# Optimization experiments

Hardware: AMD Instinct MI355X
Metric: run time of the kernel (lower is better)

The kernel has to match this reference:

```python
import jax, jax.numpy as jnp
import numpy as np

N_NODES = 50000
N_EDGES = 800000
N_FEAT = 100
HIDDEN = 100
N_CLASSES = 2
N_GRAPHS = 256


def setup_inputs() -> dict:
    key = jax.random.key(0)
    ks = jax.random.split(key, 16)
    x = jax.random.normal(ks[0], (N_NODES, N_FEAT), dtype=jnp.float32)
    edge_index = jax.random.randint(ks[1], (2, N_EDGES), 0, N_NODES, dtype=jnp.int64)
    batch = jnp.sort(jax.random.randint(ks[2], (N_NODES,), 0, N_GRAPHS, dtype=jnp.int64))
    def lin(k, fan_in, fan_out):
        s = 1.0 / np.sqrt(fan_in)
        return jax.random.uniform(k, (fan_in, fan_out), jnp.float32, -s, s)
    return {
        "x": x, "edge_index": edge_index, "batch": batch,
        # SAGEConv1: lin_l (neighbor aggr, with bias), lin_r (root, no bias)
        "W1l": lin(ks[3], N_FEAT, HIDDEN), "b1": jnp.zeros((HIDDEN,), jnp.float32), "W1r": lin(ks[4], N_FEAT, HIDDEN),
        "W2l": lin(ks[5], HIDDEN, HIDDEN), "b2": jnp.zeros((HIDDEN,), jnp.float32), "W2r": lin(ks[6], HIDDEN, HIDDEN),
        "W3l": lin(ks[7], HIDDEN, HIDDEN), "b3": jnp.zeros((HIDDEN,), jnp.float32), "W3r": lin(ks[8], HIDDEN, HIDDEN),
        "Wlin": lin(ks[9], HIDDEN, N_CLASSES), "blin": jnp.zeros((N_CLASSES,), jnp.float32),
    }


def _sage_conv(x, src, dst, Wl, b, Wr):
    # PyG SAGEConv with mean aggregation: out = lin_l(mean_{j in N(i)} x_j) + lin_r(x_i)
    msg = x[src]  # [E, d] gather
    s = jax.ops.segment_sum(msg, dst, num_segments=x.shape[0])  # [N, d]
    cnt = jax.ops.segment_sum(jnp.ones_like(dst, dtype=x.dtype), dst, num_segments=x.shape[0])
    aggr = s / jnp.maximum(cnt, 1.0)[:, None]
    return aggr @ Wl + b + x @ Wr


def reference(x, edge_index, batch, W1l, b1, W1r, W2l, b2, W2r, W3l, b3, W3r, Wlin, blin):
    src, dst = edge_index[0], edge_index[1]
    h = jax.nn.relu(_sage_conv(x, src, dst, W1l, b1, W1r))
    h = jax.nn.relu(_sage_conv(h, src, dst, W2l, b2, W2r))
    h = _sage_conv(h, src, dst, W3l, b3, W3r)
    # global_mean_pool over batch ids
    gs = jax.ops.segment_sum(h, batch, num_segments=N_GRAPHS)
    gc = jax.ops.segment_sum(jnp.ones_like(batch, dtype=h.dtype), batch, num_segments=N_GRAPHS)
    g = gs / jnp.maximum(gc, 1.0)[:, None]
    # dropout(p=0.5) is identity in eval mode
    return g @ Wlin + blin
```

## Files before the change

kernel.cpp:

```cpp
#include <hip/hip_runtime.h>
#include <hip/hip_bf16.h>

typedef __attribute__((ext_vector_type(8))) short short8v;
typedef __attribute__((ext_vector_type(4))) float f32x4;

#define PST 128
#define PSTL 136
#define MAXBUCK 1024

static __device__ inline unsigned short f2bf(float x) {
    union { float f; unsigned int u; } c; c.f = x;
    unsigned int r = (c.u + 0x7FFFu + ((c.u >> 16) & 1u)) >> 16;
    return (unsigned short)r;
}
static __device__ inline float bf2f(unsigned short h) {
    union { float f; unsigned int u; } c; c.u = ((unsigned int)h) << 16;
    return c.f;
}
static __device__ inline f32x4 MF(short8v a, short8v b, f32x4 c) {
    return __builtin_amdgcn_mfma_f32_16x16x32_bf16(a, b, c, 0, 0, 0);
}


__global__ __launch_bounds__(256) void k_bincount(const int* __restrict__ dst,
                                                  int* __restrict__ bcnt,
                                                  int n, int nbuck, int chunk) {
    __shared__ int lcnt[MAXBUCK];
    int t = threadIdx.x;
    for (int b = t; b < nbuck; b += 256) lcnt[b] = 0;
    __syncthreads();
    int e0 = blockIdx.x * chunk;
    int e1 = e0 + chunk; if (e1 > n) e1 = n;
    for (int e = e0 + t; e < e1; e += 256) atomicAdd(&lcnt[dst[e] >> 8], 1);
    __syncthreads();
    for (int b = t; b < nbuck; b += 256)
        if (lcnt[b]) atomicAdd(&bcnt[b], lcnt[b]);
}

__global__ __launch_bounds__(1024) void k_binscan(const int* __restrict__ bcnt,
                                                  int* __restrict__ bbase,
                                                  int* __restrict__ bcur,
                                                  int* __restrict__ rowp,
                                                  int nbuck, int n_nodes, int n_edges) {
    __shared__ int tmp[1024];
    int t = threadIdx.x;
    int v = (t < nbuck) ? bcnt[t] : 0;
    tmp[t] = v;
    __syncthreads();
    for (int off = 1; off < 1024; off <<= 1) {
        int u = 0;
        if (t >= off) u = tmp[t - off];
        __syncthreads();
        if (t >= off) tmp[t] += u;
        __syncthreads();
    }
    if (t < nbuck) { int b = tmp[t] - v; bbase[t] = b; bcur[t] = b; }
    if (t == 0) rowp[n_nodes] = n_edges;
}

__global__ __launch_bounds__(256) void k_binscatter(const int* __restrict__ src,
                                                    const int* __restrict__ dst,
                                                    int* __restrict__ bcur,
                                                    int* __restrict__ tmpv,
                                                    int n, int nbuck, int chunk) {
    __shared__ int lcnt[MAXBUCK];
    __shared__ int lbase[MAXBUCK];
    int t = threadIdx.x;
    for (int b = t; b < nbuck; b += 256) lcnt[b] = 0;
    __syncthreads();
    int e0 = blockIdx.x * chunk;
    int e1 = e0 + chunk; if (e1 > n) e1 = n;
    for (int e = e0 + t; e < e1; e += 256) atomicAdd(&lcnt[dst[e] >> 8], 1);
    __syncthreads();
    for (int b = t; b < nbuck; b += 256) {
        int c = lcnt[b];
        lbase[b] = c ? atomicAdd(&bcur[b], c) : 0;
        lcnt[b] = 0;
    }
    __syncthreads();
    for (int e = e0 + t; e < e1; e += 256) {
        int d = dst[e];
        int b = d >> 8;
        int r = atomicAdd(&lcnt[b], 1);
        tmpv[lbase[b] + r] = (src[e] << 8) | (d & 255);
    }
}

__global__ __launch_bounds__(256) void k_build(const int* __restrict__ tmpv,
                                               const int* __restrict__ bbase,
                                               int* __restrict__ rowp,
                                               float* __restrict__ inv,
                                               int* __restrict__ ssrc,
                                               int n_nodes, int n_edges, int nbuck) {
    __shared__ int hist[256];
    __shared__ int scan[256];
    __shared__ int curs[256];
    int b = blockIdx.x;
    int t = threadIdx.x;
    int s = bbase[b];
    int e = (b + 1 < nbuck) ? bbase[b + 1] : n_edges;
    hist[t] = 0;
    __syncthreads();
    for (int i = s + t; i < e; i += 256) atomicAdd(&hist[tmpv[i] & 255], 1);
    __syncthreads();
    int v = hist[t];
    scan[t] = v;
    __syncthreads();
    for (int off = 1; off < 256; off <<= 1) {
        int u = 0;
        if (t >= off) u = scan[t - off];
        __syncthreads();
        if (t >= off) scan[t] += u;
        __syncthreads();
    }
    int excl = scan[t] - v;
    curs[t] = excl;
    int node = (b << 8) + t;
    if (node < n_nodes) {
        rowp[node] = s + excl;
        inv[node] = 1.0f / (float)(v > 1 ? v : 1);
    }
    __syncthreads();
    for (int i = s + t; i < e; i += 256) {
        int p = tmpv[i];
        int r = atomicAdd(&curs[p & 255], 1);
        ssrc[s + r] = p >> 8;
    }
}

__global__ __launch_bounds__(256) void k_cvt(const float* __restrict__ X,
                                             unsigned short* __restrict__ Xhi,
                                             unsigned short* __restrict__ Xlo,
                                             int n) {
    int grp = threadIdx.x >> 4, l = threadIdx.x & 15;
    int i = blockIdx.x * 16 + grp;
    if (i >= n) return;
    unsigned short* ph = Xhi + (size_t)i * PST + l * 8;
    unsigned short* pl = Xlo + (size_t)i * PST + l * 8;
    if (l < 13) {
        float4 v0 = *(const float4*)(X + (size_t)i * 100 + l * 8);
        float4 v1 = (l < 12) ? *(const float4*)(X + (size_t)i * 100 + l * 8 + 4)
                             : make_float4(0.f, 0.f, 0.f, 0.f);
        float f[8] = {v0.x, v0.y, v0.z, v0.w, v1.x, v1.y, v1.z, v1.w};
        short8v hv, lv;
#pragma unroll
        for (int m = 0; m < 8; ++m) {
            unsigned short h = f2bf(f[m]);
            hv[m] = (short)h;
            lv[m] = (short)f2bf(f[m] - bf2f(h));
        }
        *(short8v*)ph = hv;
        *(short8v*)pl = lv;
    } else {
        short8v z = (short8v){0,0,0,0,0,0,0,0};
        *(short8v*)ph = z;
        *(short8v*)pl = z;
    }
}

#define PACKN (2 * 4 * 7 * 64)
__global__ __launch_bounds__(256) void k_pack3(const float* __restrict__ W1l, const float* __restrict__ W1r,
                                               const float* __restrict__ W2l, const float* __restrict__ W2r,
                                               const float* __restrict__ W3l, const float* __restrict__ W3r,
                                               unsigned short* __restrict__ B1h, unsigned short* __restrict__ B1l,
                                               unsigned short* __restrict__ B2h, unsigned short* __restrict__ B2l,
                                               unsigned short* __restrict__ B3h, unsigned short* __restrict__ B3l) {
    int gid = blockIdx.x * 256 + threadIdx.x;
    if (gid >= 3 * PACKN) return;
    int layer = gid / PACKN;
    int idx = gid - layer * PACKN;
    const float* Wl = layer == 0 ? W1l : (layer == 1 ? W2l : W3l);
    const float* Wr = layer == 0 ? W1r : (layer == 1 ? W2r : W3r);
    unsigned short* Bh = layer == 0 ? B1h : (layer == 1 ? B2h : B3h);
    unsigned short* Bl = layer == 0 ? B1l : (layer == 1 ? B2l : B3l);
    int lane = idx & 63;
    int t = idx >> 6;
    int nt = t % 7;
    int pc = t / 7;
    int part = pc >> 2, c = pc & 3;
    int col = nt * 16 + (lane & 15);
    int fbase = c * 32 + (lane >> 4) * 8;
    const float* W = part ? Wr : Wl;
    for (int jj = 0; jj < 8; ++jj) {
        int k = fbase + jj;
        float w = (k < 100 && col < 100) ? W[k * 100 + col] : 0.f;
        unsigned short h = f2bf(w);
        Bh[(size_t)idx * 8 + jj] = h;
        Bl[(size_t)idx * 8 + jj] = f2bf(w - bf2f(h));
    }
}

__global__ __launch_bounds__(128) void k_layer(const unsigned short* __restrict__ Xhi,
                                               const unsigned short* __restrict__ Xlo,
                                               const int* __restrict__ ssrc,
                                               const int* __restrict__ rowp,
                                               const float* __restrict__ inv,
                                               const unsigned short* __restrict__ Bh,
                                               const unsigned short* __restrict__ Bl,
                                               const float* __restrict__ bias,
                                               unsigned short* __restrict__ Ohi,
                                               unsigned short* __restrict__ Olo,
                                               int relu, int n) {
    __shared__ unsigned short lds_h[32][PSTL];
    __shared__ unsigned short lds_l[32][PSTL];
    const int t = threadIdx.x;
    const int wv = t >> 6;
    const int lane = t & 63;
    const int base = blockIdx.x * 32;

    {
        const int grp = lane >> 4, l = lane & 15;
        const bool act = l < 13;
        const size_t loff = (size_t)l * 8;
        const short8v z = (short8v){0,0,0,0,0,0,0,0};
#pragma unroll
        for (int it = 0; it < 4; ++it) {
            const int lr = wv * 16 + it * 4 + grp;
            const int node = base + lr;
            if (node < n) {
                int s = rowp[node];
                int e = rowp[node + 1];
                float a[8];
#pragma unroll
                for (int m = 0; m < 8; ++m) a[m] = 0.f;
                int i = s;
                for (; i + 4 <= e; i += 4) {
                    int s0 = ssrc[i], s1 = ssrc[i + 1], s2 = ssrc[i + 2], s3 = ssrc[i + 3];
                    if (act) {
                        short8v v0 = *(const short8v*)(Xhi + (size_t)s0 * PST + loff);
                        short8v v1 = *(const short8v*)(Xhi + (size_t)s1 * PST + loff);
                        short8v v2 = *(const short8v*)(Xhi + (size_t)s2 * PST + loff);
                        short8v v3 = *(const short8v*)(Xhi + (size_t)s3 * PST + loff);
#pragma unroll
                        for (int m = 0; m < 8; ++m)
                            a[m] += bf2f((unsigned short)v0[m]) + bf2f((unsigned short)v1[m])
                                  + bf2f((unsigned short)v2[m]) + bf2f((unsigned short)v3[m]);
                    }
                }
                for (; i < e; ++i) {
                    int s0 = ssrc[i];
                    if (act) {
                        short8v v0 = *(const short8v*)(Xhi + (size_t)s0 * PST + loff);
#pragma unroll
                        for (int m = 0; m < 8; ++m) a[m] += bf2f((unsigned short)v0[m]);
                    }
                }
                if (act) {
                    const float f = inv[node];
                    short8v hv, lv;
#pragma unroll
                    for (int m = 0; m < 8; ++m) {
                        float v = a[m] * f;
                        unsigned short h = f2bf(v);
                        hv[m] = (short)h;
                        lv[m] = (short)f2bf(v - bf2f(h));
                    }
                    *(short8v*)&lds_h[lr][l * 8] = hv;
                    *(short8v*)&lds_l[lr][l * 8] = lv;
                } else {
                    *(short8v*)&lds_h[lr][l * 8] = z;
                    *(short8v*)&lds_l[lr][l * 8] = z;
                }
            } else {
                *(short8v*)&lds_h[lr][l * 8] = z;
                *(short8v*)&lds_l[lr][l * 8] = z;
            }
        }
    }
    __builtin_amdgcn_wave_barrier();

    const int m0 = base + wv * 16;
    const int lrow = lane & 15;
    const int lg = lane >> 4;
    const int ldr = wv * 16 + lrow;

    f32x4 acc[7];
#pragma unroll
    for (int nt = 0; nt < 7; ++nt) acc[nt] = (f32x4){0.f, 0.f, 0.f, 0.f};

    int r0 = m0 + lrow; if (r0 >= n) r0 = n - 1;
    const size_t b0 = (size_t)r0 * PST + lg * 8;

#pragma unroll
    for (int c = 0; c < 4; ++c) {
        short8v ah0 = *(const short8v*)&lds_h[ldr][c * 32 + lg * 8];
        short8v al0 = *(const short8v*)&lds_l[ldr][c * 32 + lg * 8];
        const unsigned short* bph = Bh + ((size_t)(c * 7) * 64 + lane) * 8;
        const unsigned short* bpl = Bl + ((size_t)(c * 7) * 64 + lane) * 8;
#pragma unroll
        for (int nt = 0; nt < 7; ++nt) {
            short8v bh = *(const short8v*)(bph + nt * 512);
            short8v bl = *(const short8v*)(bpl + nt * 512);
            acc[nt] = MF(ah0, bh, acc[nt]);
            acc[nt] = MF(ah0, bl, acc[nt]);
            acc[nt] = MF(al0, bh, acc[nt]);
        }
    }
#pragma unroll
    for (int c = 0; c < 4; ++c) {
        short8v ah0 = *(const short8v*)(Xhi + b0 + c * 32);
        short8v al0 = *(const short8v*)(Xlo + b0 + c * 32);
        const unsigned short* bph = Bh + ((size_t)((4 + c) * 7) * 64 + lane) * 8;
        const unsigned short* bpl = Bl + ((size_t)((4 + c) * 7) * 64 + lane) * 8;
#pragma unroll
        for (int nt = 0; nt < 7; ++nt) {
            short8v bh = *(const short8v*)(bph + nt * 512);
            short8v bl = *(const short8v*)(bpl + nt * 512);
            acc[nt] = MF(ah0, bh, acc[nt]);
            acc[nt] = MF(ah0, bl, acc[nt]);
            acc[nt] = MF(al0, bh, acc[nt]);
        }
    }

#pragma unroll
    for (int nt = 0; nt < 7; ++nt) {
        int col = nt * 16 + lrow;
        bool cok = col < 100;
        float bb = cok ? bias[col] : 0.f;
#pragma unroll
        for (int r = 0; r < 4; ++r) {
            int row = m0 + lg * 4 + r;
            if (cok && row < n) {
                float v = acc[nt][r] + bb;
                if (relu) v = fmaxf(v, 0.f);
                unsigned short h = f2bf(v);
                size_t o = (size_t)row * PST + col;
                Ohi[o] = h;
                Olo[o] = f2bf(v - bf2f(h));
            }
        }
    }
    if (lane < 32) {
        int row = m0 + (lane >> 1);
        if (row < n) {
            unsigned short* op = ((lane & 1) == 0 ? Ohi : Olo) + (size_t)row * PST;
            short4 z4 = {0, 0, 0, 0};
            short8v z = (short8v){0,0,0,0,0,0,0,0};
            *(short4*)(op + 100) = z4;
            *(short8v*)(op + 104) = z;
            *(short8v*)(op + 112) = z;
            *(short8v*)(op + 120) = z;
        }
    }
}

__global__ __launch_bounds__(256) void k_pool(const unsigned short* __restrict__ Hhi,
                                              const unsigned short* __restrict__ Hlo,
                                              const int* __restrict__ batch,
                                              const float* __restrict__ Wlin,
                                              const float* __restrict__ blin,
                                              float* __restrict__ out, int n) {
    int g = blockIdx.x;
    int t = threadIdx.x;
    int grp = t >> 4, l = t & 15;
    int lo = 0, hi = n;
    while (lo < hi) { int m = (lo + hi) >> 1; if (batch[m] < g) lo = m + 1; else hi = m; }
    int lo2 = lo, hi2 = n;
    while (lo2 < hi2) { int m = (lo2 + hi2) >> 1; if (batch[m] < g + 1) lo2 = m + 1; else hi2 = m; }

    const bool act = l < 13;
    float a[8];
#pragma unroll
    for (int m = 0; m < 8; ++m) a[m] = 0.f;
    const size_t loff = (size_t)l * 8;
    for (int node = lo + grp; node < lo2; node += 16) {
        if (act) {
            short8v vh = *(const short8v*)(Hhi + (size_t)node * PST + loff);
            short8v vl = *(const short8v*)(Hlo + (size_t)node * PST + loff);
#pragma unroll
            for (int m = 0; m < 8; ++m)
                a[m] += bf2f((unsigned short)vh[m]) + bf2f((unsigned short)vl[m]);
        }
    }

    __shared__ float part[16][13][8];
    if (act) {
#pragma unroll
        for (int m = 0; m < 8; ++m) part[grp][l][m] = a[m];
    }
    __syncthreads();

    __shared__ float gm[104];
    if (t < 104) {
        int fg = t >> 3, m = t & 7;
        float s = 0.f;
#pragma unroll
        for (int q = 0; q < 16; ++q) s += part[q][fg][m];
        float f = (lo2 > lo) ? 1.0f / (float)(lo2 - lo) : 0.0f;
        gm[t] = s * f;
    }
    __syncthreads();
    if (t < 2) {
        float o = blin[t];
        for (int k = 0; k < 100; ++k) o += gm[k] * Wlin[k * 2 + t];
        out[g * 2 + t] = o;
    }
}


extern "C" void kernel_launch(void* const* d_in, const int* in_sizes, int n_in,
                              void* d_out, int out_size, void* d_ws, size_t ws_size,
                              hipStream_t stream) {
    const float* x    = (const float*)d_in[0];
    const int*   ei   = (const int*)d_in[1];
    const int*   batch= (const int*)d_in[2];
    const float* W1l  = (const float*)d_in[3];
    const float* b1   = (const float*)d_in[4];
    const float* W1r  = (const float*)d_in[5];
    const float* W2l  = (const float*)d_in[6];
    const float* b2   = (const float*)d_in[7];
    const float* W2r  = (const float*)d_in[8];
    const float* W3l  = (const float*)d_in[9];
    const float* b3   = (const float*)d_in[10];
    const float* W3r  = (const float*)d_in[11];
    const float* Wlin = (const float*)d_in[12];
    const float* blin = (const float*)d_in[13];
    float* out = (float*)d_out;

    const int n_nodes  = in_sizes[0] / 100;
    const int n_edges  = in_sizes[1] / 2;
    const int n_graphs = out_size / 2;
    const int* src = ei;
    const int* dst = ei + n_edges;

    char* ws = (char*)d_ws;
    size_t o = 0;
    auto alloc = [&](size_t bytes) { size_t r = o; o = (o + bytes + 255) & ~(size_t)255; return r; };
    int*   rowp = (int*)(ws + alloc((size_t)(n_nodes + 1) * 4));
    float* inv  = (float*)(ws + alloc((size_t)n_nodes * 4));
    int*   ssrc = (int*)(ws + alloc((size_t)n_edges * 4));
    int*   bcnt = (int*)(ws + alloc(MAXBUCK * 4));
    int*   bbase= (int*)(ws + alloc(MAXBUCK * 4));
    int*   bcur = (int*)(ws + alloc(MAXBUCK * 4));
    int*   tmpv = (int*)(ws + alloc((size_t)n_edges * 4));
    const size_t pbytes = (size_t)n_nodes * PST * 2;
    unsigned short* XAhi = (unsigned short*)(ws + alloc(pbytes));
    unsigned short* XAlo = (unsigned short*)(ws + alloc(pbytes));
    unsigned short* XBhi = (unsigned short*)(ws + alloc(pbytes));
    unsigned short* XBlo = (unsigned short*)(ws + alloc(pbytes));
    const size_t bfb = (size_t)PACKN * 8 * 2;
    unsigned short* B1h = (unsigned short*)(ws + alloc(bfb));
    unsigned short* B1l = (unsigned short*)(ws + alloc(bfb));
    unsigned short* B2h = (unsigned short*)(ws + alloc(bfb));
    unsigned short* B2l = (unsigned short*)(ws + alloc(bfb));
    unsigned short* B3h = (unsigned short*)(ws + alloc(bfb));
    unsigned short* B3l = (unsigned short*)(ws + alloc(bfb));

    hipMemsetAsync(bcnt, 0, MAXBUCK * 4, stream);

    const int nbuck = (n_nodes + 255) >> 8;
    const int chunk = (n_edges + 255) / 256;

    k_bincount<<<256, 256, 0, stream>>>(dst, bcnt, n_edges, nbuck, chunk);
    k_binscan<<<1, 1024, 0, stream>>>(bcnt, bbase, bcur, rowp, nbuck, n_nodes, n_edges);
    k_binscatter<<<256, 256, 0, stream>>>(src, dst, bcur, tmpv, n_edges, nbuck, chunk);
    k_build<<<nbuck, 256, 0, stream>>>(tmpv, bbase, rowp, inv, ssrc,
                                       n_nodes, n_edges, nbuck);

    k_pack3<<<(3 * PACKN + 255) / 256, 256, 0, stream>>>(
        W1l, W1r, W2l, W2r, W3l, W3r, B1h, B1l, B2h, B2l, B3h, B3l);

    const int nb16 = (n_nodes + 15) / 16;
    const int lgrid = (n_nodes + 31) / 32;

    k_cvt<<<nb16, 256, 0, stream>>>(x, XAhi, XAlo, n_nodes);

    k_layer<<<lgrid, 128, 0, stream>>>(XAhi, XAlo, ssrc, rowp, inv, B1h, B1l, b1,
                                       XBhi, XBlo, 1, n_nodes);
    k_layer<<<lgrid, 128, 0, stream>>>(XBhi, XBlo, ssrc, rowp, inv, B2h, B2l, b2,
                                       XAhi, XAlo, 1, n_nodes);
    k_layer<<<lgrid, 128, 0, stream>>>(XAhi, XAlo, ssrc, rowp, inv, B3h, B3l, b3,
                                       XBhi, XBlo, 0, n_nodes);

    k_pool<<<n_graphs, 256, 0, stream>>>(XBhi, XBlo, batch, Wlin, blin, out, n_nodes);
}
```

Before: 236.7 us.

## Split layer block work across waves by edge halves and output column tiles

Each block now handles 16 nodes instead of 32. The two waves each gather half of every node's edge range and write fp32 partial sums to LDS. After a block barrier the partials are summed, scaled and split into bf16 hi/lo. The MFMA GEMM is then split by output columns, with wave 0 computing 4 column tiles and wave 1 computing 3. This doubles the grid and cuts per-wave serial work, aiming for better latency hiding. In exchange it adds a __syncthreads, an uneven column split, and each B fragment is now loaded by one wave per 16 rows instead of per 32.

New measurement: 267.0 us. 1.13x slower.

```diff
diff --git a/kernel.cpp b/kernel.cpp
--- a/kernel.cpp
+++ b/kernel.cpp
@@ -5,7 +5,6 @@
 typedef __attribute__((ext_vector_type(4))) float f32x4;
 
 #define PST 128
-#define PSTL 136
 #define MAXBUCK 1024
 
 static __device__ inline unsigned short f2bf(float x) {
@@ -190,6 +189,71 @@
     }
 }
 
+template<int NTB, int NTN>
+static __device__ inline void mfma_store(const short8v (&pah)[4], const short8v (&pal)[4],
+                                         const unsigned short* __restrict__ Xhi,
+                                         const unsigned short* __restrict__ Xlo,
+                                         size_t b0,
+                                         const unsigned short* __restrict__ Bh,
+                                         const unsigned short* __restrict__ Bl,
+                                         const float* __restrict__ bias,
+                                         unsigned short* __restrict__ Ohi,
+                                         unsigned short* __restrict__ Olo,
+                                         int relu, int n, int m0, int lane) {
+    const int lrow = lane & 15;
+    const int lg = lane >> 4;
+    f32x4 acc[NTN];
+#pragma unroll
+    for (int nt = 0; nt < NTN; ++nt) acc[nt] = (f32x4){0.f, 0.f, 0.f, 0.f};
+
+#pragma unroll
+    for (int c = 0; c < 4; ++c) {
+        const unsigned short* bph = Bh + ((size_t)(c * 7 + NTB) * 64 + lane) * 8;
+        const unsigned short* bpl = Bl + ((size_t)(c * 7 + NTB) * 64 + lane) * 8;
+#pragma unroll
+        for (int nt = 0; nt < NTN; ++nt) {
+            short8v bh = *(const short8v*)(bph + nt * 512);
+            short8v bl = *(const short8v*)(bpl + nt * 512);
+            acc[nt] = MF(pah[c], bh, acc[nt]);
+            acc[nt] = MF(pah[c], bl, acc[nt]);
+            acc[nt] = MF(pal[c], bh, acc[nt]);
+        }
+    }
+#pragma unroll
+    for (int c = 0; c < 4; ++c) {
+        short8v xh = *(const short8v*)(Xhi + b0 + c * 32);
+        short8v xl = *(const short8v*)(Xlo + b0 + c * 32);
+        const unsigned short* bph = Bh + ((size_t)((4 + c) * 7 + NTB) * 64 + lane) * 8;
+        const unsigned short* bpl = Bl + ((size_t)((4 + c) * 7 + NTB) * 64 + lane) * 8;
+#pragma unroll
+        for (int nt = 0; nt < NTN; ++nt) {
+            short8v bh = *(const short8v*)(bph + nt * 512);
+            short8v bl = *(const short8v*)(bpl + nt * 512);
+            acc[nt] = MF(xh, bh, acc[nt]);
+            acc[nt] = MF(xh, bl, acc[nt]);
+            acc[nt] = MF(xl, bh, acc[nt]);
+        }
+    }
+#pragma unroll
+    for (int nt = 0; nt < NTN; ++nt) {
+        int col = (NTB + nt) * 16 + lrow;
+        bool cok = col < 100;
+        float bb = cok ? bias[col] : 0.f;
+#pragma unroll
+        for (int r = 0; r < 4; ++r) {
+            int row = m0 + lg * 4 + r;
+            if (cok && row < n) {
+                float v = acc[nt][r] + bb;
+                if (relu) v = fmaxf(v, 0.f);
+                unsigned short h = f2bf(v);
+                size_t o = (size_t)row * PST + col;
+                Ohi[o] = h;
+                Olo[o] = f2bf(v - bf2f(h));
+            }
+        }
+    }
+}
+
 __global__ __launch_bounds__(128) void k_layer(const unsigned short* __restrict__ Xhi,
                                                const unsigned short* __restrict__ Xlo,
                                                const int* __restrict__ ssrc,
@@ -201,29 +265,28 @@
                                                unsigned short* __restrict__ Ohi,
                                                unsigned short* __restrict__ Olo,
                                                int relu, int n) {
-    __shared__ unsigned short lds_h[32][PSTL];
-    __shared__ unsigned short lds_l[32][PSTL];
+    __shared__ float pa[2][16][104];
     const int t = threadIdx.x;
     const int wv = t >> 6;
     const int lane = t & 63;
-    const int base = blockIdx.x * 32;
+    const int base = blockIdx.x * 16;
 
     {
         const int grp = lane >> 4, l = lane & 15;
         const bool act = l < 13;
         const size_t loff = (size_t)l * 8;
-        const short8v z = (short8v){0,0,0,0,0,0,0,0};
 #pragma unroll
         for (int it = 0; it < 4; ++it) {
-            const int lr = wv * 16 + it * 4 + grp;
+            const int lr = it * 4 + grp;
             const int node = base + lr;
+            float a[8];
+#pragma unroll
+            for (int m = 0; m < 8; ++m) a[m] = 0.f;
             if (node < n) {
                 int s = rowp[node];
-                int e = rowp[node + 1];
-                float a[8];
-#pragma unroll
-                for (int m = 0; m < 8; ++m) a[m] = 0.f;
-                int i = s;
+                int deg = rowp[node + 1] - s;
+                int i = s + ((deg * wv) >> 1);
+                int e = s + ((deg * (wv + 1)) >> 1);
                 for (; i + 4 <= e; i += 4) {
                     int s0 = ssrc[i], s1 = ssrc[i + 1], s2 = ssrc[i + 2], s3 = ssrc[i + 3];
                     if (act) {
@@ -245,93 +308,52 @@
                         for (int m = 0; m < 8; ++m) a[m] += bf2f((unsigned short)v0[m]);
                     }
                 }
-                if (act) {
-                    const float f = inv[node];
-                    short8v hv, lv;
-#pragma unroll
-                    for (int m = 0; m < 8; ++m) {
-                        float v = a[m] * f;
-                        unsigned short h = f2bf(v);
-                        hv[m] = (short)h;
-                        lv[m] = (short)f2bf(v - bf2f(h));
-                    }
-                    *(short8v*)&lds_h[lr][l * 8] = hv;
-                    *(short8v*)&lds_l[lr][l * 8] = lv;
-                } else {
-                    *(short8v*)&lds_h[lr][l * 8] = z;
-                    *(short8v*)&lds_l[lr][l * 8] = z;
-                }
-            } else {
-                *(short8v*)&lds_h[lr][l * 8] = z;
-                *(short8v*)&lds_l[lr][l * 8] = z;
             }
-        }
-    }
-    __builtin_amdgcn_wave_barrier();
-
-    const int m0 = base + wv * 16;
+            if (act) {
+                *(float4*)&pa[wv][lr][l * 8] = make_float4(a[0], a[1], a[2], a[3]);
+                *(float4*)&pa[wv][lr][l * 8 + 4] = make_float4(a[4], a[5], a[6], a[7]);
+            }
+        }
+    }
+    __syncthreads();
+
     const int lrow = lane & 15;
     const int lg = lane >> 4;
-    const int ldr = wv * 16 + lrow;
-
-    f32x4 acc[7];
-#pragma unroll
-    for (int nt = 0; nt < 7; ++nt) acc[nt] = (f32x4){0.f, 0.f, 0.f, 0.f};
-
-    int r0 = m0 + lrow; if (r0 >= n) r0 = n - 1;
+    int r0 = base + lrow; if (r0 >= n) r0 = n - 1;
     const size_t b0 = (size_t)r0 * PST + lg * 8;
-
+    const float fin = inv[r0];
+
+    short8v pah[4], pal[4];
 #pragma unroll
     for (int c = 0; c < 4; ++c) {
-        short8v ah0 = *(const short8v*)&lds_h[ldr][c * 32 + lg * 8];
-        short8v al0 = *(const short8v*)&lds_l[ldr][c * 32 + lg * 8];
-        const unsigned short* bph = Bh + ((size_t)(c * 7) * 64 + lane) * 8;
-        const unsigned short* bpl = Bl + ((size_t)(c * 7) * 64 + lane) * 8;
-#pragma unroll
-        for (int nt = 0; nt < 7; ++nt) {
-            short8v bh = *(const short8v*)(bph + nt * 512);
-            short8v bl = *(const short8v*)(bpl + nt * 512);
-            acc[nt] = MF(ah0, bh, acc[nt]);
-            acc[nt] = MF(ah0, bl, acc[nt]);
-            acc[nt] = MF(al0, bh, acc[nt]);
-        }
-    }
-#pragma unroll
-    for (int c = 0; c < 4; ++c) {
-        short8v ah0 = *(const short8v*)(Xhi + b0 + c * 32);
-        short8v al0 = *(const short8v*)(Xlo + b0 + c * 32);
-        const unsigned short* bph = Bh + ((size_t)((4 + c) * 7) * 64 + lane) * 8;
-        const unsigned short* bpl = Bl + ((size_t)((4 + c) * 7) * 64 + lane) * 8;
-#pragma unroll
-        for (int nt = 0; nt < 7; ++nt) {
-            short8v bh = *(const short8v*)(bph + nt * 512);
-            short8v bl = *(const short8v*)(bpl + nt * 512);
-            acc[nt] = MF(ah0, bh, acc[nt]);
-            acc[nt] = MF(ah0, bl, acc[nt]);
-            acc[nt] = MF(al0, bh, acc[nt]);
-        }
-    }
-
-#pragma unroll
-    for (int nt = 0; nt < 7; ++nt) {
-        int col = nt * 16 + lrow;
-        bool cok = col < 100;
-        float bb = cok ? bias[col] : 0.f;
-#pragma unroll
-        for (int r = 0; r < 4; ++r) {
-            int row = m0 + lg * 4 + r;
-            if (cok && row < n) {
-                float v = acc[nt][r] + bb;
-                if (relu) v = fmaxf(v, 0.f);
-                unsigned short h = f2bf(v);
-                size_t o = (size_t)row * PST + col;
-                Ohi[o] = h;
-                Olo[o] = f2bf(v - bf2f(h));
+        const int idx = c * 32 + lg * 8;
+        short8v ah = (short8v){0,0,0,0,0,0,0,0};
+        short8v al = (short8v){0,0,0,0,0,0,0,0};
+        if (idx < 104) {
+            float4 a0 = *(const float4*)&pa[0][lrow][idx];
+            float4 a1 = *(const float4*)&pa[0][lrow][idx + 4];
+            float4 b0v = *(const float4*)&pa[1][lrow][idx];
+            float4 b1v = *(const float4*)&pa[1][lrow][idx + 4];
+            float v[8] = {a0.x + b0v.x, a0.y + b0v.y, a0.z + b0v.z, a0.w + b0v.w,
+                          a1.x + b1v.x, a1.y + b1v.y, a1.z + b1v.z, a1.w + b1v.w};
+#pragma unroll
+            for (int m = 0; m < 8; ++m) {
+                float vv = v[m] * fin;
+                unsigned short h = f2bf(vv);
+                ah[m] = (short)h;
+                al[m] = (short)f2bf(vv - bf2f(h));
             }
         }
-    }
-    if (lane < 32) {
-        int row = m0 + (lane >> 1);
+        pah[c] = ah; pal[c] = al;
+    }
+
+    if (wv == 0)
+        mfma_store<0, 4>(pah, pal, Xhi, Xlo, b0, Bh, Bl, bias, Ohi, Olo, relu, n, base, lane);
+    else
+        mfma_store<4, 3>(pah, pal, Xhi, Xlo, b0, Bh, Bl, bias, Ohi, Olo, relu, n, base, lane);
+
+    if (wv == 1 && lane < 32) {
+        int row = base + (lane >> 1);
         if (row < n) {
             unsigned short* op = ((lane & 1) == 0 ? Ohi : Olo) + (size_t)row * PST;
             short4 z4 = {0, 0, 0, 0};
@@ -461,16 +483,15 @@
         W1l, W1r, W2l, W2r, W3l, W3r, B1h, B1l, B2h, B2l, B3h, B3l);
 
     const int nb16 = (n_nodes + 15) / 16;
-    const int lgrid = (n_nodes + 31) / 32;
 
     k_cvt<<<nb16, 256, 0, stream>>>(x, XAhi, XAlo, n_nodes);
 
-    k_layer<<<lgrid, 128, 0, stream>>>(XAhi, XAlo, ssrc, rowp, inv, B1h, B1l, b1,
-                                       XBhi, XBlo, 1, n_nodes);
-    k_layer<<<lgrid, 128, 0, stream>>>(XBhi, XBlo, ssrc, rowp, inv, B2h, B2l, b2,
-                                       XAhi, XAlo, 1, n_nodes);
-    k_layer<<<lgrid, 128, 0, stream>>>(XAhi, XAlo, ssrc, rowp, inv, B3h, B3l, b3,
-                                       XBhi, XBlo, 0, n_nodes);
+    k_layer<<<nb16, 128, 0, stream>>>(XAhi, XAlo, ssrc, rowp, inv, B1h, B1l, b1,
+                                      XBhi, XBlo, 1, n_nodes);
+    k_layer<<<nb16, 128, 0, stream>>>(XBhi, XBlo, ssrc, rowp, inv, B2h, B2l, b2,
+                                      XAhi, XAlo, 1, n_nodes);
+    k_layer<<<nb16, 128, 0, stream>>>(XAhi, XAlo, ssrc, rowp, inv, B3h, B3l, b3,
+                                      XBhi, XBlo, 0, n_nodes);
 
     k_pool<<<n_graphs, 256, 0, stream>>>(XBhi, XBlo, batch, Wlin, blin, out, n_nodes);
 }
```
